# Kernel optimization log

Hardware: AMD Instinct MI355X
Metric: run time of the kernel (lower is better)

## Reference

```python
import jax, jax.numpy as jnp
import numpy as np
from itertools import combinations

B, J, D, H, L, DFF = 2048, 7, 128, 8, 4, 512
TH, GH = 4, 4  # triplet cross-attn heads (min(4,128//32)), group-transformer heads

def _build_static():
    trips = list(combinations(range(J), 3))
    tid = {t: i for i, t in enumerate(trips)}
    member = np.zeros((J, len(trips)), dtype=bool)
    for i, t in enumerate(trips):
        for j in t:
            member[j, i] = True
    isr_l, g1_l, g2_l = [], [], []
    for isr in range(J):
        rem = [j for j in range(J) if j != isr]
        for c in combinations(rem, 3):
            comp = tuple(j for j in rem if j not in c)
            if c < comp:
                isr_l.append(isr); g1_l.append(c); g2_l.append(comp)
    return (np.array(trips), member, np.array(isr_l), np.array(g1_l), np.array(g2_l),
            np.array([tid[t] for t in g1_l]), np.array([tid[t] for t in g2_l]))

TRIPS, MEMBER, ISR_IDX, G1_JETS, G2_JETS, G1_TID, G2_TID = _build_static()
N_ASSIGN = len(ISR_IDX)  # 70
TCA_MASK = np.where(MEMBER, 0.0, -1e9).astype(np.float32)  # (J, 35) jet-restricted mask

def _gelu(x):
    return jax.nn.gelu(x, approximate=False)

def _ln(x, g, b, eps=1e-5):
    mu = x.mean(-1, keepdims=True)
    v = ((x - mu) ** 2).mean(-1, keepdims=True)
    return (x - mu) / jnp.sqrt(v + eps) * g + b

def _attend(q, k, v, nhead, bias=None):
    Bq, Lq, d = q.shape
    Lk = k.shape[1]
    dh = d // nhead
    qh = q.reshape(Bq, Lq, nhead, dh)
    kh = k.reshape(Bq, Lk, nhead, dh)
    vh = v.reshape(Bq, Lk, nhead, dh)
    s = jnp.einsum('bqhd,bkhd->bhqk', qh, kh) / np.float32(np.sqrt(dh))
    if bias is not None:
        s = s + bias
    a = jax.nn.softmax(s, -1)
    return jnp.einsum('bhqk,bkhd->bqhd', a, vh).reshape(Bq, Lq, d)

def _enc_layer(x, Wqkv, bqkv, Wo, bo, g1, b1, g2, b2, W1, bb1, W2, bb2, nhead, bias=None):
    # pre-LN TransformerEncoderLayer (norm_first=True, relu activation, eval mode)
    h = _ln(x, g1, b1)
    q, k, v = jnp.split(h @ Wqkv + bqkv, 3, axis=-1)
    x = x + _attend(q, k, v, nhead, bias) @ Wo + bo
    h2 = _ln(x, g2, b2)
    return x + jax.nn.relu(h2 @ W1 + bb1) @ W2 + bb2

def _feat6(p):
    E, px, py, pz = p[..., 0], p[..., 1], p[..., 2], p[..., 3]
    pt = jnp.sqrt(px ** 2 + py ** 2)
    p3 = jnp.sqrt(pt ** 2 + pz ** 2)
    m = jnp.sqrt(jnp.maximum(E ** 2 - p3 ** 2, 1e-8))
    eta = jnp.arcsinh(pz / jnp.maximum(pt, 1e-8))
    phi = jnp.arctan2(py, px)
    return jnp.stack([m, pt, eta, phi, E, p3], -1)

def _forward(four_momenta, W_in, b_in, pt_w, dr_w, mass_w, enc_Wqkv, enc_bqkv, enc_Wo, enc_bo, enc_g1, enc_b1, enc_g2, enc_b2, enc_W1, enc_bb1, enc_W2, enc_bb2, tca_Wq, tca_bq, tca_Wk, tca_bk, tca_Wv, tca_bv, tca_Wo, tca_bo, tca_g1, tca_b1, tca_W1, tca_bb1, tca_W2, tca_bb2, tca_g2, tca_b2, gt_Wqkv, gt_bqkv, gt_Wo, gt_bo, gt_g1, gt_b1, gt_g2, gt_b2, gt_W1, gt_bb1, gt_W2, gt_bb2, ph_g, ph_b, s_W1, s_b1, s_W2, s_b2, s_W3, s_b3):
    fm = four_momenta
    E, px, py, pz = fm[..., 0], fm[..., 1], fm[..., 2], fm[..., 3]
    pt = jnp.maximum(jnp.sqrt(px ** 2 + py ** 2), 1e-8)
    log_pt = jnp.log(pt)
    eta = jnp.arcsinh(pz / pt)
    phi = jnp.arctan2(py, px)
    m_jet = jnp.sqrt(jnp.maximum(E ** 2 - px ** 2 - py ** 2 - pz ** 2, 1e-8))
    x = jnp.concatenate([fm, jnp.stack([log_pt, eta, phi, m_jet], -1)], -1) @ W_in + b_in

    # fused per-head additive attention biases: pT hierarchy, deltaR, pair invariant mass
    pt_b = log_pt[:, :, None] - log_pt[:, None, :]
    cphi, sphi = px / pt, py / pt
    deta = eta[:, :, None] - eta[:, None, :]
    cdphi = jnp.clip(cphi[:, :, None] * cphi[:, None, :] + sphi[:, :, None] * sphi[:, None, :], -1.0 + 1e-7, 1.0 - 1e-7)
    dr_b = jnp.sqrt(deta ** 2 + jnp.arccos(cdphi) ** 2)
    Es = E[:, :, None] + E[:, None, :]
    ps2 = (px[:, :, None] + px[:, None, :]) ** 2 + (py[:, :, None] + py[:, None, :]) ** 2 + (pz[:, :, None] + pz[:, None, :]) ** 2
    mass_b = 0.5 * jnp.log(jnp.maximum(Es ** 2 - ps2, 1e-8))
    bias = (pt_w[None, :, None, None] * pt_b[:, None] + dr_w[None, :, None, None] * dr_b[:, None] + mass_w[None, :, None, None] * mass_b[:, None])  # (B,H,J,J)

    for i in range(L):
        x = _enc_layer(x, enc_Wqkv[i], enc_bqkv[i], enc_Wo[i], enc_bo[i], enc_g1[i], enc_b1[i], enc_g2[i], enc_b2[i], enc_W1[i], enc_bb1[i], enc_W2[i], enc_bb2[i], H, bias)
    jet_emb = x  # (B, J, D)

    # jet-restricted triplet cross-attention over the C(7,3)=35 triplet bank
    triplet_emb = jet_emb[:, TRIPS].mean(2)  # (B, 35, D)
    q = jet_emb @ tca_Wq + tca_bq
    k = triplet_emb @ tca_Wk + tca_bk
    v = triplet_emb @ tca_Wv + tca_bv
    attn = _attend(q, k, v, TH, jnp.asarray(TCA_MASK)[None, None]) @ tca_Wo + tca_bo
    jet_emb = _ln(jet_emb + attn, tca_g1, tca_b1)
    ff = _gelu(jet_emb @ tca_W1 + tca_bb1) @ tca_W2 + tca_bb2
    jet_emb = _ln(jet_emb + ff, tca_g2, tca_b2)

    # GroupTransformer over all unique 3-jet groups in parallel, mean-pool readout
    nT = len(TRIPS)
    gt_in = jet_emb[:, TRIPS].reshape(B * nT, 3, D)
    gt_out = _enc_layer(gt_in, gt_Wqkv, gt_bqkv, gt_Wo, gt_bo, gt_g1, gt_b1, gt_g2, gt_b2, gt_W1, gt_bb1, gt_W2, gt_bb2, GH)
    group_emb = gt_out.mean(1).reshape(B, nT, D)  # (B, 35, D)

    g1e = group_emb[:, G1_TID]  # (B, 70, D)
    g2e = group_emb[:, G2_TID]
    pair_sum = g1e + g2e
    pair_prod = g1e * g2e
    pair_sqdiff = (g1e - g2e) ** 2
    isr_emb = jet_emb[:, ISR_IDX]  # (B, 70, D)
    event_emb = jnp.broadcast_to(jet_emb.mean(1)[:, None], (B, N_ASSIGN, D))

    p_g1 = fm[:, G1_JETS].sum(2)  # (B, 70, 4)
    p_g2 = fm[:, G2_JETS].sum(2)
    p_isr = fm[:, ISR_IDX]
    physics = jnp.concatenate([_feat6(p_g1), _feat6(p_g2), _feat6(p_isr), _feat6(p_g1 + p_g2)], -1)  # (B,70,24)
    physics = _ln(physics, ph_g, ph_b)

    feats = jnp.concatenate([isr_emb, pair_sum, pair_prod, pair_sqdiff, event_emb, physics], -1)  # (B,70,5D+24)
    h = _gelu(feats @ s_W1 + s_b1)
    h = _gelu(h @ s_W2 + s_b2)
    return (h @ s_W3 + s_b3)[..., 0]  # (B, 70) assignment logits


def setup_inputs():
    key = jax.random.key(0)
    ks = iter(jax.random.split(key, 100))
    def nrm(shape, s=0.02):
        return jax.random.normal(next(ks), shape, jnp.float32) * s
    p3 = jax.random.normal(next(ks), (B, J, 3), jnp.float32) * 50.0
    mm = jnp.abs(jax.random.normal(next(ks), (B, J), jnp.float32)) * 20.0 + 5.0
    E = jnp.sqrt((p3 ** 2).sum(-1) + mm ** 2)
    d = {'four_momenta': jnp.concatenate([E[..., None], p3], -1)}
    d.update(W_in=nrm((8, D)), b_in=jnp.zeros((D,)),
             pt_w=nrm((H,), 0.1), dr_w=nrm((H,), 0.1), mass_w=nrm((H,), 0.1),
             enc_Wqkv=nrm((L, D, 3 * D)), enc_bqkv=jnp.zeros((L, 3 * D)),
             enc_Wo=nrm((L, D, D)), enc_bo=jnp.zeros((L, D)),
             enc_g1=jnp.ones((L, D)), enc_b1=jnp.zeros((L, D)),
             enc_g2=jnp.ones((L, D)), enc_b2=jnp.zeros((L, D)),
             enc_W1=nrm((L, D, DFF)), enc_bb1=jnp.zeros((L, DFF)),
             enc_W2=nrm((L, DFF, D)), enc_bb2=jnp.zeros((L, D)),
             tca_Wq=nrm((D, D)), tca_bq=jnp.zeros((D,)),
             tca_Wk=nrm((D, D)), tca_bk=jnp.zeros((D,)),
             tca_Wv=nrm((D, D)), tca_bv=jnp.zeros((D,)),
             tca_Wo=nrm((D, D)), tca_bo=jnp.zeros((D,)),
             tca_g1=jnp.ones((D,)), tca_b1=jnp.zeros((D,)),
             tca_W1=nrm((D, 2 * D)), tca_bb1=jnp.zeros((2 * D,)),
             tca_W2=nrm((2 * D, D)), tca_bb2=jnp.zeros((D,)),
             tca_g2=jnp.ones((D,)), tca_b2=jnp.zeros((D,)),
             gt_Wqkv=nrm((D, 3 * D)), gt_bqkv=jnp.zeros((3 * D,)),
             gt_Wo=nrm((D, D)), gt_bo=jnp.zeros((D,)),
             gt_g1=jnp.ones((D,)), gt_b1=jnp.zeros((D,)),
             gt_g2=jnp.ones((D,)), gt_b2=jnp.zeros((D,)),
             gt_W1=nrm((D, 2 * D)), gt_bb1=jnp.zeros((2 * D,)),
             gt_W2=nrm((2 * D, D)), gt_bb2=jnp.zeros((D,)),
             ph_g=jnp.ones((24,)), ph_b=jnp.zeros((24,)),
             s_W1=nrm((5 * D + 24, 2 * D)), s_b1=jnp.zeros((2 * D,)),
             s_W2=nrm((2 * D, D)), s_b2=jnp.zeros((D,)),
             s_W3=nrm((D, 1)), s_b3=jnp.zeros((1,)))
    return d


def reference(four_momenta, W_in, b_in, pt_w, dr_w, mass_w, enc_Wqkv, enc_bqkv, enc_Wo, enc_bo, enc_g1, enc_b1, enc_g2, enc_b2, enc_W1, enc_bb1, enc_W2, enc_bb2, tca_Wq, tca_bq, tca_Wk, tca_bk, tca_Wv, tca_bv, tca_Wo, tca_bo, tca_g1, tca_b1, tca_W1, tca_bb1, tca_W2, tca_bb2, tca_g2, tca_b2, gt_Wqkv, gt_bqkv, gt_Wo, gt_bo, gt_g1, gt_b1, gt_g2, gt_b2, gt_W1, gt_bb1, gt_W2, gt_bb2, ph_g, ph_b, s_W1, s_b1, s_W2, s_b2, s_W3, s_b3):
    return _forward(four_momenta, W_in, b_in, pt_w, dr_w, mass_w, enc_Wqkv, enc_bqkv, enc_Wo, enc_bo, enc_g1, enc_b1, enc_g2, enc_b2, enc_W1, enc_bb1, enc_W2, enc_bb2, tca_Wq, tca_bq, tca_Wk, tca_bk, tca_Wv, tca_bv, tca_Wo, tca_bo, tca_g1, tca_b1, tca_W1, tca_bb1, tca_W2, tca_bb2, tca_g2, tca_b2, gt_Wqkv, gt_bqkv, gt_Wo, gt_bo, gt_g1, gt_b1, gt_g2, gt_b2, gt_W1, gt_bb1, gt_W2, gt_bb2, ph_g, ph_b, s_W1, s_b1, s_W2, s_b2, s_W3, s_b3)
```

## Files before the change

kernel.cpp:

```cpp
#include <hip/hip_runtime.h>
#include <hip/hip_bf16.h>
#include <math.h>

typedef __hip_bfloat16 bf16;

constexpr int NB=2048, NJ=7, ND=128, NHD=8, NLYR=4, NFF=512, NTR=35, NAS=70;
constexpr int SD=132, S256=260, S384=388, S512=516;

struct KArgs { const void* p[54]; void* out; const void* flag; };

__device__ __forceinline__ float bfbits(unsigned short s){ return __uint_as_float(((unsigned)s)<<16); }
__device__ __forceinline__ float ldv(const float* p, size_t i){ return p[i]; }
__device__ __forceinline__ float ldv(const bf16* p, size_t i){ return __bfloat162float(p[i]); }
__device__ __forceinline__ void ldv4(const float* p, size_t i, float* o){
  const float4 v=*reinterpret_cast<const float4*>(p+i);
  o[0]=v.x; o[1]=v.y; o[2]=v.z; o[3]=v.w;
}
__device__ __forceinline__ void ldv4(const bf16* p, size_t i, float* o){
  unsigned long long u=*reinterpret_cast<const unsigned long long*>((const unsigned short*)p+i);
  o[0]=bfbits((unsigned short)u);
  o[1]=bfbits((unsigned short)(u>>16));
  o[2]=bfbits((unsigned short)(u>>32));
  o[3]=bfbits((unsigned short)(u>>48));
}
__device__ __forceinline__ void stv(float* p, size_t i, float v){ p[i]=v; }
__device__ __forceinline__ void stv(bf16* p, size_t i, float v){ p[i]=__float2bfloat16(v); }
__device__ __forceinline__ float gelu_f(float x){ return 0.5f*x*(1.0f+erff(x*0.70710678118654752f)); }

__device__ void build_trips(int* tr){
  int n=0;
  for(int a=0;a<NJ;a++)for(int b=a+1;b<NJ;b++)for(int c=b+1;c<NJ;c++){
    tr[n*3+0]=a; tr[n*3+1]=b; tr[n*3+2]=c; n++;
  }
}
__device__ int find_tid(const int* tr,int a,int b,int c){
  for(int t=0;t<NTR;t++) if(tr[t*3]==a&&tr[t*3+1]==b&&tr[t*3+2]==c) return t;
  return 0;
}
__device__ void build_assign(const int* tr,int* isr,int* g1t,int* g2t,int* g1j,int* g2j){
  int n=0;
  for(int is=0;is<NJ;is++){
    int rem[6],m=0;
    for(int j=0;j<NJ;j++) if(j!=is) rem[m++]=j;
    for(int i=0;i<6;i++)for(int jj=i+1;jj<6;jj++)for(int k=jj+1;k<6;k++){
      int c0=rem[i],c1=rem[jj],c2=rem[k];
      int comp[3],q=0;
      for(int r=0;r<6;r++){ int v=rem[r]; if(v!=c0&&v!=c1&&v!=c2) comp[q++]=v; }
      bool lt=(c0<comp[0])||(c0==comp[0]&&(c1<comp[1]||(c1==comp[1]&&c2<comp[2])));
      if(lt){
        isr[n]=is;
        g1j[n*3]=c0; g1j[n*3+1]=c1; g1j[n*3+2]=c2;
        g2j[n*3]=comp[0]; g2j[n*3+1]=comp[1]; g2j[n*3+2]=comp[2];
        g1t[n]=find_tid(tr,c0,c1,c2);
        g2t[n]=find_tid(tr,comp[0],comp[1],comp[2]);
        n++;
      }
    }
  }
}

template<typename T>
__device__ void lnr(const float* src, int ASs, float* dst, int ASd, const T* g, const T* bb,
                    float* mu, float* rs, int rows, int tid, int NT){
  for(int r0=0;r0<rows;r0+=(NT>>5)){
    int row=r0+(tid>>5), lane=tid&31;
    if(row<rows){
      const float* s=src+row*ASs;
      float m=0.f,v=0.f;
      for(int d=lane;d<ND;d+=32){ float t=s[d]; m+=t; v+=t*t; }
      for(int off=16;off>0;off>>=1){ m+=__shfl_down(m,off,32); v+=__shfl_down(v,off,32); }
      if(lane==0){ m*=(1.f/ND); float vv=v*(1.f/ND)-m*m; mu[row]=m; rs[row]=rsqrtf(fmaxf(vv,0.f)+1e-5f); }
    }
    __syncthreads();
  }
  for(int idx=tid; idx<rows*ND; idx+=NT){
    int j=idx>>7, d=idx&127;
    dst[j*ASd+d]=(src[j*ASs+d]-mu[j])*rs[j]*ldv(g,d)+ldv(bb,d);
  }
  __syncthreads();
}

template<typename T>
__device__ void mm4b(const float* a, int ASa, const T* W, const T* bias, float* out, int ASo,
                     int M, int K, int N, int tid, int NT, int act, bool accum, int RB){
  int NQ=N>>2;
  int CGS=NT/RB;
  if(tid<CGS*RB){
    int i=tid%RB, cg0=tid/RB;
    if(i<M){
      const float* ar=a+i*ASa;
      for(int cg=cg0; cg<NQ; cg+=CGS){
        int k4=cg<<2;
        float acc[4];
        if(bias) ldv4(bias,k4,acc);
        else { acc[0]=0.f;acc[1]=0.f;acc[2]=0.f;acc[3]=0.f; }
        for(int d=0; d<K; d++){
          float w[4]; ldv4(W,(size_t)d*N+k4,w);
          float av=ar[d];
          acc[0]+=av*w[0]; acc[1]+=av*w[1]; acc[2]+=av*w[2]; acc[3]+=av*w[3];
        }
        int o=i*ASo+k4;
        #pragma unroll
        for(int j=0;j<4;j++){
          float v=acc[j];
          if(act==1) v=fmaxf(v,0.f); else if(act==2) v=gelu_f(v);
          if(accum) out[o+j]+=v; else out[o+j]=v;
        }
      }
    }
  }
  __syncthreads();
}

__global__ void k_detect(const unsigned short* w, int n, unsigned* flag){
  __shared__ int bad[256];
  int tid=threadIdx.x;
  int my=0;
  for(int i=tid;i<n;i+=256){
    unsigned e=(w[i]>>7)&0xFFu;
    if(e>=134u) my=1;
  }
  bad[tid]=my;
  __syncthreads();
  if(tid==0){
    int any=0; for(int i=0;i<256;i++) any|=bad[i];
    flag[0]= any?1u:0u;
  }
}


template<typename T>
__device__ void phase_embed(const T* fm, const T* Win, const T* bin,
                            const T* ptw, const T* drw, const T* mw,
                            float* xS, float* biasS, float* scratch, int b, int tid, int NT){
  float* fE =scratch+0;  float* fpx=scratch+8;  float* fpy=scratch+16; float* fpz=scratch+24;
  float* flp=scratch+32; float* fet=scratch+40; float* fcp=scratch+48; float* fsp=scratch+56;
  float* fph=scratch+64; float* fms=scratch+72;
  if(tid<NJ){
    size_t base=((size_t)b*NJ+tid)*4;
    float e=ldv(fm,base+0), x_=ldv(fm,base+1), y_=ldv(fm,base+2), z_=ldv(fm,base+3);
    float pt=fmaxf(sqrtf(x_*x_+y_*y_),1e-8f);
    fE[tid]=e; fpx[tid]=x_; fpy[tid]=y_; fpz[tid]=z_;
    flp[tid]=logf(pt);
    fet[tid]=asinhf(z_/pt);
    fph[tid]=atan2f(y_,x_);
    fms[tid]=sqrtf(fmaxf(e*e-x_*x_-y_*y_-z_*z_,1e-8f));
    fcp[tid]=x_/pt; fsp[tid]=y_/pt;
  }
  __syncthreads();
  for(int idx=tid; idx<NJ*ND; idx+=NT){
    int j=idx>>7, d=idx&127;
    float in8[8]={fE[j],fpx[j],fpy[j],fpz[j],flp[j],fet[j],fph[j],fms[j]};
    float acc=ldv(bin,d);
    for(int c=0;c<8;c++) acc += in8[c]*ldv(Win,c*ND+d);
    xS[j*SD+d]=acc;
  }
  for(int idx=tid; idx<NHD*NJ*NJ; idx+=NT){
    int h=idx/49, r=idx%49, i=r/7, jj=r%7;
    float ptb=flp[i]-flp[jj];
    float deta=fet[i]-fet[jj];
    float cd=fcp[i]*fcp[jj]+fsp[i]*fsp[jj];
    cd=fminf(fmaxf(cd,-1.0f+1e-7f),1.0f-1e-7f);
    float ac=acosf(cd);
    float dr=sqrtf(deta*deta+ac*ac);
    float Es=fE[i]+fE[jj];
    float sx=fpx[i]+fpx[jj], sy=fpy[i]+fpy[jj], sz=fpz[i]+fpz[jj];
    float mb=0.5f*logf(fmaxf(Es*Es-(sx*sx+sy*sy+sz*sz),1e-8f));
    biasS[idx]=ldv(ptw,h)*ptb+ldv(drw,h)*dr+ldv(mw,h)*mb;
  }
  __syncthreads();
}

template<typename T>
__device__ void phase_enc(float* xS, const float* biasS, float* P, float* muS, float* rsS,
    const T* eWqkv,const T* ebqkv,const T* eWo,const T* ebo,
    const T* eg1,const T* eb1,const T* eg2,const T* eb2,
    const T* eW1,const T* ebb1,const T* eW2,const T* ebb2, int tid, int NT){
  float* h  =P+0;
  float* qkv=P+924;
  float* att=P+3640;
  float* sb =P+4564;
  float* ff =P+924;
  for(int l=0;l<NLYR;l++){
    lnr(xS,SD,h,SD,eg1+l*ND,eb1+l*ND,muS,rsS,NJ,tid,NT);
    mm4b(h,SD,eWqkv+(size_t)l*ND*3*ND,ebqkv+l*3*ND,qkv,S384,NJ,ND,3*ND,tid,NT,0,false,8);
    for(int idx=tid;idx<NHD*NJ*NJ;idx+=NT){
      int hh=idx/49, r=idx%49, i=r/7, jj=r%7;
      float acc=0.f;
      const float* qr=&qkv[i*S384+hh*16];
      const float* kr=&qkv[jj*S384+128+hh*16];
      for(int d=0;d<16;d++) acc+=qr[d]*kr[d];
      sb[idx]=acc*0.25f+biasS[idx];
    }
    __syncthreads();
    if(tid<NHD*NJ){
      float* s=&sb[tid*7];
      float mx=s[0]; for(int j=1;j<7;j++) mx=fmaxf(mx,s[j]);
      float sm=0.f; for(int j=0;j<7;j++){ s[j]=expf(s[j]-mx); sm+=s[j]; }
      float inv=1.0f/sm; for(int j=0;j<7;j++) s[j]*=inv;
    }
    __syncthreads();
    for(int idx=tid;idx<NJ*ND;idx+=NT){
      int i=idx>>7, d=idx&127, hh=d>>4;
      float acc=0.f;
      for(int j=0;j<7;j++) acc+=sb[(hh*7+i)*7+j]*qkv[j*S384+256+d];
      att[i*SD+d]=acc;
    }
    __syncthreads();
    mm4b(att,SD,eWo+(size_t)l*ND*ND,ebo+l*ND,xS,SD,NJ,ND,ND,tid,NT,0,true,8);
    lnr(xS,SD,h,SD,eg2+l*ND,eb2+l*ND,muS,rsS,NJ,tid,NT);
    mm4b(h,SD,eW1+(size_t)l*ND*NFF,ebb1+l*NFF,ff,S512,NJ,ND,NFF,tid,NT,1,false,8);
    mm4b(ff,S512,eW2+(size_t)l*NFF*ND,ebb2+l*ND,xS,SD,NJ,NFF,ND,tid,NT,0,true,8);
  }
}

template<typename T>
__device__ void trip_proj(const float* xS, const int* trS, const T* W, const T* bias,
                          float* out, int tid, int NT){
  int CGS=NT>>3;
  for(int base=0;base<NTR;base+=8){
    int t=base+(tid&7);
    if(t<NTR){
      int a0=trS[t*3]*SD, a1=trS[t*3+1]*SD, a2=trS[t*3+2]*SD;
      for(int cg=tid>>3; cg<32; cg+=CGS){
        int k4=cg<<2;
        float acc[4]; ldv4(bias,k4,acc);
        for(int c=0;c<ND;c++){
          float tv=(xS[a0+c]+xS[a1+c]+xS[a2+c])*(1.0f/3.0f);
          float w[4]; ldv4(W,(size_t)c*ND+k4,w);
          acc[0]+=tv*w[0]; acc[1]+=tv*w[1]; acc[2]+=tv*w[2]; acc[3]+=tv*w[3];
        }
        int o=t*SD+k4;
        out[o]=acc[0]; out[o+1]=acc[1]; out[o+2]=acc[2]; out[o+3]=acc[3];
      }
    }
  }
  __syncthreads();
}

template<typename T>
__device__ void phase_tca(float* xS, float* P, float* muS, float* rsS, const int* trS,
    const T* tWq,const T* tbq,const T* tWk,const T* tbk,const T* tWv,const T* tbv,
    const T* tWo,const T* tbo,const T* tg1,const T* tb1,const T* tW1,const T* tbb1,
    const T* tW2,const T* tbb2,const T* tg2,const T* tb2, int tid, int NT){
  float* q   =P+0;
  float* kv  =P+924;
  float* sb4 =P+5544;
  float* att2=P+6524;
  float* tff =P+0;
  const float sc=0.17677669529663687f;
  mm4b(xS,SD,tWq,tbq,q,SD,NJ,ND,ND,tid,NT,0,false,8);
  trip_proj(xS,trS,tWk,tbk,kv,tid,NT);
  for(int idx=tid;idx<4*NJ*NTR;idx+=NT){
    int hh=idx/245, r=idx%245, i=r/35, t=r%35;
    float acc=0.f;
    const float* qr=&q[i*SD+hh*32];
    const float* kr=&kv[t*SD+hh*32];
    for(int d=0;d<32;d++) acc+=qr[d]*kr[d];
    bool mem=(trS[t*3]==i||trS[t*3+1]==i||trS[t*3+2]==i);
    sb4[idx]=acc*sc+(mem?0.0f:-1e9f);
  }
  __syncthreads();
  if(tid<4*NJ){
    float* s=&sb4[tid*35];
    float mx=-3e38f; for(int t=0;t<35;t++) mx=fmaxf(mx,s[t]);
    float sm=0.f; for(int t=0;t<35;t++){ s[t]=expf(s[t]-mx); sm+=s[t]; }
    float inv=1.0f/sm; for(int t=0;t<35;t++) s[t]*=inv;
  }
  __syncthreads();
  trip_proj(xS,trS,tWv,tbv,kv,tid,NT);
  for(int idx=tid;idx<NJ*ND;idx+=NT){
    int i=idx>>7, d=idx&127, hh=d>>5;
    float acc=0.f;
    for(int t=0;t<35;t++) acc+=sb4[(hh*7+i)*35+t]*kv[t*SD+d];
    att2[i*SD+d]=acc;
  }
  __syncthreads();
  mm4b(att2,SD,tWo,tbo,xS,SD,NJ,ND,ND,tid,NT,0,true,8);
  lnr(xS,SD,xS,SD,tg1,tb1,muS,rsS,NJ,tid,NT);
  mm4b(xS,SD,tW1,tbb1,tff,S256,NJ,ND,2*ND,tid,NT,2,false,8);
  mm4b(tff,S256,tW2,tbb2,xS,SD,NJ,2*ND,ND,tid,NT,0,true,8);
  lnr(xS,SD,xS,SD,tg2,tb2,muS,rsS,NJ,tid,NT);
}


template<typename T>
__global__ __launch_bounds__(256) void k_front(KArgs A, unsigned want, float* X2, float* EVT){
  if(((const unsigned*)A.flag)[0]!=want) return;
  int b=blockIdx.x, tid=threadIdx.x;
  __shared__ float xS[NJ*SD];
  __shared__ float biasS[NHD*NJ*NJ];
  __shared__ float P[7448];
  __shared__ float muS[16], rsS[16];
  __shared__ int trS[NTR*3];
  if(tid==0) build_trips(trS);
  __syncthreads();
  phase_embed((const T*)A.p[0],(const T*)A.p[1],(const T*)A.p[2],
              (const T*)A.p[3],(const T*)A.p[4],(const T*)A.p[5],xS,biasS,P,b,tid,256);
  phase_enc(xS,biasS,P,muS,rsS,
    (const T*)A.p[6],(const T*)A.p[7],(const T*)A.p[8],(const T*)A.p[9],
    (const T*)A.p[10],(const T*)A.p[11],(const T*)A.p[12],(const T*)A.p[13],
    (const T*)A.p[14],(const T*)A.p[15],(const T*)A.p[16],(const T*)A.p[17],tid,256);
  phase_tca(xS,P,muS,rsS,trS,
    (const T*)A.p[18],(const T*)A.p[19],(const T*)A.p[20],(const T*)A.p[21],
    (const T*)A.p[22],(const T*)A.p[23],(const T*)A.p[24],(const T*)A.p[25],
    (const T*)A.p[26],(const T*)A.p[27],(const T*)A.p[28],(const T*)A.p[29],
    (const T*)A.p[30],(const T*)A.p[31],(const T*)A.p[32],(const T*)A.p[33],tid,256);
  for(int idx=tid;idx<NJ*ND;idx+=256) X2[(size_t)b*NJ*ND+idx]=xS[(idx>>7)*SD+(idx&127)];
  if(tid<ND){
    float s=0.f; for(int j=0;j<NJ;j++) s+=xS[j*SD+tid];
    EVT[(size_t)b*ND+tid]=s*(1.0f/NJ);
  }
}

template<typename T>
__global__ __launch_bounds__(256) void k_gt(KArgs A, unsigned want, const float* X2, float* GRP){
  if(((const unsigned*)A.flag)[0]!=want) return;
  const T* gWqkv=(const T*)A.p[34]; const T* gbqkv=(const T*)A.p[35];
  const T* gWo  =(const T*)A.p[36]; const T* gbo  =(const T*)A.p[37];
  const T* gg1  =(const T*)A.p[38]; const T* gb1  =(const T*)A.p[39];
  const T* gg2  =(const T*)A.p[40]; const T* gb2  =(const T*)A.p[41];
  const T* gW1  =(const T*)A.p[42]; const T* gbb1 =(const T*)A.p[43];
  const T* gW2  =(const T*)A.p[44]; const T* gbb2 =(const T*)A.p[45];
  int b=blockIdx.x/12, ch=blockIdx.x%12, tid=threadIdx.x;
  int c0=ch*3, tc=(NTR-c0)<3?(NTR-c0):3;
  int ntok=3*tc;
  __shared__ float jets[NJ*SD];
  __shared__ float xg[9*SD];
  __shared__ float hg[9*SD];
  __shared__ float qkvg[9*S384];
  __shared__ float sbg[108];
  __shared__ float muS[16], rsS[16];
  __shared__ int trS[NTR*3];
  if(tid==0) build_trips(trS);
  for(int idx=tid;idx<NJ*ND;idx+=256) jets[(idx>>7)*SD+(idx&127)]=X2[(size_t)b*NJ*ND+idx];
  __syncthreads();
  const float sc=0.17677669529663687f;
  for(int idx=tid;idx<ntok*ND;idx+=256){
    int s=idx>>7, d=idx&127; int t=c0+s/3, r=s%3;
    xg[s*SD+d]=jets[trS[t*3+r]*SD+d];
  }
  __syncthreads();
  lnr(xg,SD,hg,SD,gg1,gb1,muS,rsS,ntok,tid,256);
  mm4b(hg,SD,gWqkv,gbqkv,qkvg,S384,ntok,ND,3*ND,tid,256,0,false,9);
  for(int idx=tid;idx<tc*36;idx+=256){
    int s=idx/36, r=idx%36, hh=r/9, p=r%9, i=p/3, j=p%3;
    float acc=0.f;
    const float* qr=&qkvg[(s*3+i)*S384+hh*32];
    const float* kr=&qkvg[(s*3+j)*S384+128+hh*32];
    for(int d=0;d<32;d++) acc+=qr[d]*kr[d];
    sbg[idx]=acc*sc;
  }
  __syncthreads();
  for(int q2=tid;q2<tc*12;q2+=256){
    int s=q2/12, r2=q2%12;
    float* base=&sbg[s*36+(r2/3)*9+(r2%3)*3];
    float mx=fmaxf(base[0],fmaxf(base[1],base[2]));
    float e0=expf(base[0]-mx),e1=expf(base[1]-mx),e2=expf(base[2]-mx);
    float inv=1.0f/(e0+e1+e2);
    base[0]=e0*inv; base[1]=e1*inv; base[2]=e2*inv;
  }
  __syncthreads();
  for(int idx=tid;idx<ntok*ND;idx+=256){
    int sr=idx>>7, d=idx&127; int s=sr/3, i=sr%3, hh=d>>5;
    float acc=0.f;
    for(int j=0;j<3;j++) acc+=sbg[s*36+hh*9+i*3+j]*qkvg[(s*3+j)*S384+256+d];
    hg[sr*SD+d]=acc;
  }
  __syncthreads();
  mm4b(hg,SD,gWo,gbo,xg,SD,ntok,ND,ND,tid,256,0,true,9);
  lnr(xg,SD,hg,SD,gg2,gb2,muS,rsS,ntok,tid,256);
  mm4b(hg,SD,gW1,gbb1,qkvg,S256,ntok,ND,2*ND,tid,256,1,false,9);
  mm4b(qkvg,S256,gW2,gbb2,xg,SD,ntok,2*ND,ND,tid,256,0,true,9);
  for(int idx=tid;idx<tc*ND;idx+=256){
    int s=idx>>7, d=idx&127;
    GRP[((size_t)b*NTR+c0+s)*ND+d]=
      (xg[(s*3)*SD+d]+xg[(s*3+1)*SD+d]+xg[(s*3+2)*SD+d])*(1.0f/3.0f);
  }
}

template<typename T>
__global__ __launch_bounds__(512) void k_score(KArgs A, unsigned want,
    const float* X2, const float* EVT, const float* GRP){
  if(((const unsigned*)A.flag)[0]!=want) return;
  const T* fm =(const T*)A.p[0];
  const T* phg=(const T*)A.p[46]; const T* phb=(const T*)A.p[47];
  const T* sW1=(const T*)A.p[48]; const T* sb1=(const T*)A.p[49];
  const T* sW2=(const T*)A.p[50]; const T* sb2=(const T*)A.p[51];
  const T* sW3=(const T*)A.p[52]; const T* sb3=(const T*)A.p[53];
  T* OUT=(T*)A.out;
  int b=blockIdx.x, tid=threadIdx.x;
  int ar=tid&7, cg=tid>>3;

  __shared__ float POOL[12472];
  float* grpP=POOL;
  float* Ws  =POOL+4680;
  float* h2t =POOL+4680;
  float* h1c =POOL+8776;
  float* Fc  =POOL+10096;
  float* jets=POOL+10096;
  __shared__ float physAll[72*24];
  __shared__ float isrc[7*260];
  __shared__ float evtc[256];
  __shared__ float evtS[128];
  __shared__ float fmvS[28];
  __shared__ int trS[105];
  __shared__ int isrS[72], g1tS[72], g2tS[72], g1jS[216], g2jS[216];

  if(tid==0){
    build_trips(trS); build_assign(trS,isrS,g1tS,g2tS,g1jS,g2jS);
    for(int a=70;a<72;a++){
      isrS[a]=0; g1tS[a]=0; g2tS[a]=0;
      for(int r=0;r<3;r++){ g1jS[a*3+r]=0; g2jS[a*3+r]=0; }
    }
  }
  for(int idx=tid;idx<NTR*ND;idx+=512) grpP[(idx>>7)*132+(idx&127)]=GRP[(size_t)b*NTR*ND+idx];
  for(int idx=tid;idx<NJ*ND;idx+=512) jets[idx]=X2[(size_t)b*NJ*ND+idx];
  if(tid<ND) evtS[tid]=EVT[(size_t)b*ND+tid];
  if(tid>=128&&tid<128+NJ*4){ int q=tid-128; fmvS[q]=ldv(fm,(size_t)b*NJ*4+q); }
  __syncthreads();

  {
    int i=tid&7, k4=(tid>>3)<<2;
    const float* src=(i<7)?(jets+i*ND):evtS;
    size_t rb=(i<7)?0:(size_t)4*ND;
    float acc[4];
    if(i==7) ldv4(sb1,k4,acc); else { acc[0]=0.f;acc[1]=0.f;acc[2]=0.f;acc[3]=0.f; }
    for(int d=0;d<ND;d++){
      float w[4]; ldv4(sW1,(rb+d)*2*ND+k4,w);
      float av=src[d];
      acc[0]+=av*w[0]; acc[1]+=av*w[1]; acc[2]+=av*w[2]; acc[3]+=av*w[3];
    }
    if(i<7){ int o=i*260+k4; isrc[o]=acc[0]; isrc[o+1]=acc[1]; isrc[o+2]=acc[2]; isrc[o+3]=acc[3]; }
    else   { evtc[k4]=acc[0]; evtc[k4+1]=acc[1]; evtc[k4+2]=acc[2]; evtc[k4+3]=acc[3]; }
  }
  if(tid<72*4){
    int a=tid>>2, g=tid&3;
    float* o=&physAll[a*24+g*6];
    if(a<NAS){
      float p[4];
      #pragma unroll
      for(int c=0;c<4;c++){
        float v;
        if(g==0)      v=fmvS[g1jS[a*3]*4+c]+fmvS[g1jS[a*3+1]*4+c]+fmvS[g1jS[a*3+2]*4+c];
        else if(g==1) v=fmvS[g2jS[a*3]*4+c]+fmvS[g2jS[a*3+1]*4+c]+fmvS[g2jS[a*3+2]*4+c];
        else if(g==2) v=fmvS[isrS[a]*4+c];
        else          v=fmvS[g1jS[a*3]*4+c]+fmvS[g1jS[a*3+1]*4+c]+fmvS[g1jS[a*3+2]*4+c]
                       +fmvS[g2jS[a*3]*4+c]+fmvS[g2jS[a*3+1]*4+c]+fmvS[g2jS[a*3+2]*4+c];
        p[c]=v;
      }
      float E=p[0], x_=p[1], y_=p[2], z_=p[3];
      float pt=sqrtf(x_*x_+y_*y_);
      float p3=sqrtf(pt*pt+z_*z_);
      float m =sqrtf(fmaxf(E*E-p3*p3,1e-8f));
      float eta=asinhf(z_/fmaxf(pt,1e-8f));
      float ph=atan2f(y_,x_);
      o[0]=m; o[1]=pt; o[2]=eta; o[3]=ph; o[4]=E; o[5]=p3;
    } else { o[0]=0;o[1]=0;o[2]=0;o[3]=0;o[4]=0;o[5]=0; }
  }
  __syncthreads();
  if(tid<72){
    float* o=&physAll[tid*24];
    float m=0.f; for(int c=0;c<24;c++) m+=o[c]; m*=(1.0f/24.0f);
    float v=0.f; for(int c=0;c<24;c++){ float t=o[c]-m; v+=t*t; } v*=(1.0f/24.0f);
    float r=rsqrtf(v+1e-5f);
    for(int c=0;c<24;c++) o[c]=(o[c]-m)*r*ldv(phg,c)+ldv(phb,c);
  }
  __syncthreads();

  for(int t=0;t<2;t++){
    int tbase=t*40;
    int ns=(t==0)?5:4;
    float acc[5][4];
    #pragma unroll
    for(int s=0;s<5;s++){ acc[s][0]=0.f;acc[s][1]=0.f;acc[s][2]=0.f;acc[s][3]=0.f; }

    for(int kc=0;kc<408;kc+=16){
      int csz=(408-kc)<16?(408-kc):16;
      for(int idx4=tid*4; idx4<csz*256; idx4+=2048){
        int d=idx4>>8, n=idx4&255;
        int c=kc+d;
        size_t r=(c<384)? (size_t)(ND+c) : (size_t)(5*ND+(c-384));
        float w[4]; ldv4(sW1,r*2*ND+n,w);
        Ws[d*256+n]=w[0]; Ws[d*256+n+1]=w[1]; Ws[d*256+n+2]=w[2]; Ws[d*256+n+3]=w[3];
      }
      for(int idx=tid; idx<72*16; idx+=512){
        int a=idx>>4, d=idx&15;
        if(d<csz){
          int c=kc+d;
          float f;
          if(c<384){
            int cc=c&127, kind=c>>7;
            float u=grpP[g1tS[a]*132+cc], w=grpP[g2tS[a]*132+cc];
            f=(kind==0)?(u+w):(kind==1)?(u*w):(u-w)*(u-w);
          } else f=physAll[a*24+(c-384)];
          Fc[a*17+d]=f;
        }
      }
      __syncthreads();
      for(int d=0;d<csz;d++){
        float w[4]; 
        const float* wp=&Ws[d*256+(cg<<2)];
        w[0]=wp[0]; w[1]=wp[1]; w[2]=wp[2]; w[3]=wp[3];
        #pragma unroll
        for(int s=0;s<5;s++){
          if(s<ns){
            float f=Fc[(tbase+ar+8*s)*17+d];
            acc[s][0]+=f*w[0]; acc[s][1]+=f*w[1]; acc[s][2]+=f*w[2]; acc[s][3]+=f*w[3];
          }
        }
      }
      __syncthreads();
    }
    float h1r[5][4];
    #pragma unroll
    for(int s=0;s<5;s++){
      if(s<ns){
        int a=tbase+ar+8*s;
        int ir=isrS[a];
        #pragma unroll
        for(int j=0;j<4;j++){
          int k=(cg<<2)+j;
          h1r[s][j]=gelu_f(acc[s][j]+evtc[k]+isrc[ir*260+k]);
        }
      } else { h1r[s][0]=0;h1r[s][1]=0;h1r[s][2]=0;h1r[s][3]=0; }
    }

    float acc2[5][4];
    {
      float b2v[4]; int k4b=(cg&31)<<2; ldv4(sb2,k4b,b2v);
      #pragma unroll
      for(int s=0;s<5;s++){ acc2[s][0]=b2v[0];acc2[s][1]=b2v[1];acc2[s][2]=b2v[2];acc2[s][3]=b2v[3]; }
    }
    for(int fc=0;fc<256;fc+=32){
      if(cg>=(fc>>2)&&cg<(fc>>2)+8){
        int dcol=(cg<<2)-fc;
        #pragma unroll
        for(int s=0;s<5;s++){
          if(s<ns){
            int al=ar+8*s;
            h1c[al*33+dcol]  =h1r[s][0];
            h1c[al*33+dcol+1]=h1r[s][1];
            h1c[al*33+dcol+2]=h1r[s][2];
            h1c[al*33+dcol+3]=h1r[s][3];
          }
        }
      }
      for(int idx4=tid*4; idx4<32*128; idx4+=2048){
        int d=idx4>>7, n=idx4&127;
        float w[4]; ldv4(sW2,(size_t)(fc+d)*128+n,w);
        Ws[d*128+n]=w[0]; Ws[d*128+n+1]=w[1]; Ws[d*128+n+2]=w[2]; Ws[d*128+n+3]=w[3];
      }
      __syncthreads();
      if(cg<32){
        for(int d=0;d<32;d++){
          const float* wp=&Ws[d*128+(cg<<2)];
          float w0=wp[0],w1=wp[1],w2=wp[2],w3=wp[3];
          #pragma unroll
          for(int s=0;s<5;s++){
            if(s<ns){
              float f=h1c[(ar+8*s)*33+d];
              acc2[s][0]+=f*w0; acc2[s][1]+=f*w1; acc2[s][2]+=f*w2; acc2[s][3]+=f*w3;
            }
          }
        }
      }
      __syncthreads();
    }
    if(cg<32){
      int k4=cg<<2;
      #pragma unroll
      for(int s=0;s<5;s++){
        if(s<ns){
          int al=ar+8*s;
          h2t[al*129+k4]  =gelu_f(acc2[s][0]);
          h2t[al*129+k4+1]=gelu_f(acc2[s][1]);
          h2t[al*129+k4+2]=gelu_f(acc2[s][2]);
          h2t[al*129+k4+3]=gelu_f(acc2[s][3]);
        }
      }
    }
    __syncthreads();
    {
      int widx=tid>>6, lane=tid&63;
      int nal=(t==0)?40:30;
      for(int s2=0;s2<5;s2++){
        int al=widx+8*s2;
        if(al<nal){
          float part=h2t[al*129+lane]*ldv(sW3,lane)+h2t[al*129+64+lane]*ldv(sW3,64+lane);
          for(int off=32;off>0;off>>=1) part+=__shfl_down(part,off,64);
          if(lane==0) stv(OUT,(size_t)b*NAS+tbase+al,part+ldv(sb3,0));
        }
      }
    }
    __syncthreads();
  }
}

extern "C" void kernel_launch(void* const* d_in, const int* in_sizes, int n_in,
                              void* d_out, int out_size, void* d_ws, size_t ws_size,
                              hipStream_t stream){
  KArgs A;
  for(int i=0;i<54;i++) A.p[i]=d_in[i];
  A.out=d_out;
  A.flag=d_ws;

  float* ws=(float*)d_ws;
  float* X2  = ws+16;
  float* EVT = X2 + (size_t)NB*NJ*ND;
  float* GRP = EVT + (size_t)NB*ND;

  k_detect<<<1,256,0,stream>>>((const unsigned short*)d_in[1],1024,(unsigned*)d_ws);

  k_front<bf16> <<<NB,256,0,stream>>>(A,0u,X2,EVT);
  k_front<float><<<NB,256,0,stream>>>(A,1u,X2,EVT);
  k_gt<bf16>    <<<NB*12,256,0,stream>>>(A,0u,X2,GRP);
  k_gt<float>   <<<NB*12,256,0,stream>>>(A,1u,X2,GRP);
  k_score<bf16> <<<NB,512,0,stream>>>(A,0u,X2,EVT,GRP);
  k_score<float><<<NB,512,0,stream>>>(A,1u,X2,EVT,GRP);
}
```

Baseline: 7.639 ms.

## Stage weight tiles in shared memory for per-event matmuls and enlarge group-transformer chunks

Replaces the per-thread global-memory weight streaming matmul with a staged version. The block cooperatively loads K-chunks of the weight matrix into a shared buffer, and each thread then accumulates several output slots from it. Triplet projections get the same treatment. The group-transformer kernel now handles 6 triplets per block instead of 3, halving the block count so each staged weight tile is reused across more tokens. The cost is more shared memory per block, which lowers occupancy, plus extra barriers per chunk.

After: 9.998 ms. 1.31x slower.

```diff
diff --git a/kernel.cpp b/kernel.cpp
--- a/kernel.cpp
+++ b/kernel.cpp
@@ -80,33 +80,103 @@
   __syncthreads();
 }
 
-template<typename T>
-__device__ void mm4b(const float* a, int ASa, const T* W, const T* bias, float* out, int ASo,
-                     int M, int K, int N, int tid, int NT, int act, bool accum, int RB){
-  int NQ=N>>2;
-  int CGS=NT/RB;
-  if(tid<CGS*RB){
-    int i=tid%RB, cg0=tid/RB;
-    if(i<M){
-      const float* ar=a+i*ASa;
-      for(int cg=cg0; cg<NQ; cg+=CGS){
-        int k4=cg<<2;
-        float acc[4];
-        if(bias) ldv4(bias,k4,acc);
-        else { acc[0]=0.f;acc[1]=0.f;acc[2]=0.f;acc[3]=0.f; }
-        for(int d=0; d<K; d++){
-          float w[4]; ldv4(W,(size_t)d*N+k4,w);
-          float av=ar[d];
-          acc[0]+=av*w[0]; acc[1]+=av*w[1]; acc[2]+=av*w[2]; acc[3]+=av*w[3];
-        }
-        int o=i*ASo+k4;
-        #pragma unroll
-        for(int j=0;j<4;j++){
-          float v=acc[j];
-          if(act==1) v=fmaxf(v,0.f); else if(act==2) v=gelu_f(v);
-          if(accum) out[o+j]+=v; else out[o+j]=v;
-        }
-      }
+template<int N, int KC, int MAXSL, typename T>
+__device__ void mm_stage(const float* a, int ASa, const T* W, const T* bias,
+                         float* out, int ASo, int M, int K, float* Ws,
+                         int tid, int NT, int act, bool accum){
+  constexpr int NQ=N>>2;
+  int slots=M*NQ;
+  int rj[MAXSL], c4[MAXSL];
+  float acc[MAXSL][4];
+  #pragma unroll
+  for(int j=0;j<MAXSL;j++){
+    int s=tid+j*NT;
+    if(s<slots){
+      rj[j]=s%M; c4[j]=(s/M)<<2;
+      if(bias) ldv4(bias,c4[j],acc[j]);
+      else { acc[j][0]=0.f;acc[j][1]=0.f;acc[j][2]=0.f;acc[j][3]=0.f; }
+    }
+  }
+  for(int kc=0;kc<K;kc+=KC){
+    for(int i4=tid*4;i4<KC*N;i4+=NT*4){
+      int d=i4/N, n=i4-d*N;
+      float w[4]; ldv4(W,(size_t)(kc+d)*N+n,w);
+      *(float4*)&Ws[d*N+n]=make_float4(w[0],w[1],w[2],w[3]);
+    }
+    __syncthreads();
+    #pragma unroll
+    for(int j=0;j<MAXSL;j++){
+      int s=tid+j*NT;
+      if(s<slots){
+        const float* ap=a+rj[j]*ASa+kc;
+        const float* wp=Ws+c4[j];
+        for(int d=0;d<KC;d++){
+          float av=ap[d];
+          float4 wv=*(const float4*)(wp+d*N);
+          acc[j][0]+=av*wv.x; acc[j][1]+=av*wv.y; acc[j][2]+=av*wv.z; acc[j][3]+=av*wv.w;
+        }
+      }
+    }
+    __syncthreads();
+  }
+  #pragma unroll
+  for(int j=0;j<MAXSL;j++){
+    int s=tid+j*NT;
+    if(s<slots){
+      int o=rj[j]*ASo+c4[j];
+      #pragma unroll
+      for(int q=0;q<4;q++){
+        float v=acc[j][q];
+        if(act==1) v=fmaxf(v,0.f); else if(act==2) v=gelu_f(v);
+        if(accum) out[o+q]+=v; else out[o+q]=v;
+      }
+    }
+  }
+  __syncthreads();
+}
+
+template<int MAXSL, typename T>
+__device__ void mm_stage_trip(const float* xS, const int* trS, const T* W, const T* bias,
+                              float* out, float* Ws, int tid, int NT){
+  const int slots=NTR*32;
+  int a0[MAXSL],a1[MAXSL],a2[MAXSL],c4[MAXSL],tt[MAXSL];
+  float acc[MAXSL][4];
+  #pragma unroll
+  for(int j=0;j<MAXSL;j++){
+    int s=tid+j*NT;
+    if(s<slots){
+      int t=s%NTR; tt[j]=t; c4[j]=(s/NTR)<<2;
+      a0[j]=trS[t*3]*SD; a1[j]=trS[t*3+1]*SD; a2[j]=trS[t*3+2]*SD;
+      ldv4(bias,c4[j],acc[j]);
+    }
+  }
+  for(int kc=0;kc<128;kc+=16){
+    for(int i4=tid*4;i4<16*128;i4+=NT*4){
+      int d=i4>>7, n=i4&127;
+      float w[4]; ldv4(W,(size_t)(kc+d)*128+n,w);
+      *(float4*)&Ws[d*128+n]=make_float4(w[0],w[1],w[2],w[3]);
+    }
+    __syncthreads();
+    #pragma unroll
+    for(int j=0;j<MAXSL;j++){
+      int s=tid+j*NT;
+      if(s<slots){
+        const float* wp=Ws+c4[j];
+        for(int d=0;d<16;d++){
+          float tv=(xS[a0[j]+kc+d]+xS[a1[j]+kc+d]+xS[a2[j]+kc+d])*(1.0f/3.0f);
+          float4 wv=*(const float4*)(wp+d*128);
+          acc[j][0]+=tv*wv.x; acc[j][1]+=tv*wv.y; acc[j][2]+=tv*wv.z; acc[j][3]+=tv*wv.w;
+        }
+      }
+    }
+    __syncthreads();
+  }
+  #pragma unroll
+  for(int j=0;j<MAXSL;j++){
+    int s=tid+j*NT;
+    if(s<slots){
+      int o=tt[j]*SD+c4[j];
+      out[o]=acc[j][0]; out[o+1]=acc[j][1]; out[o+2]=acc[j][2]; out[o+3]=acc[j][3];
     }
   }
   __syncthreads();
@@ -172,7 +242,8 @@
 }
 
 template<typename T>
-__device__ void phase_enc(float* xS, const float* biasS, float* P, float* muS, float* rsS,
+__device__ void phase_enc(float* xS, const float* biasS, float* P, float* Ws,
+    float* muS, float* rsS,
     const T* eWqkv,const T* ebqkv,const T* eWo,const T* ebo,
     const T* eg1,const T* eb1,const T* eg2,const T* eb2,
     const T* eW1,const T* ebb1,const T* eW2,const T* ebb2, int tid, int NT){
@@ -183,7 +254,7 @@
   float* ff =P+924;
   for(int l=0;l<NLYR;l++){
     lnr(xS,SD,h,SD,eg1+l*ND,eb1+l*ND,muS,rsS,NJ,tid,NT);
-    mm4b(h,SD,eWqkv+(size_t)l*ND*3*ND,ebqkv+l*3*ND,qkv,S384,NJ,ND,3*ND,tid,NT,0,false,8);
+    mm_stage<384,16,3>(h,SD,eWqkv+(size_t)l*ND*3*ND,ebqkv+l*3*ND,qkv,S384,NJ,ND,Ws,tid,NT,0,false);
     for(int idx=tid;idx<NHD*NJ*NJ;idx+=NT){
       int hh=idx/49, r=idx%49, i=r/7, jj=r%7;
       float acc=0.f;
@@ -207,39 +278,15 @@
       att[i*SD+d]=acc;
     }
     __syncthreads();
-    mm4b(att,SD,eWo+(size_t)l*ND*ND,ebo+l*ND,xS,SD,NJ,ND,ND,tid,NT,0,true,8);
+    mm_stage<128,16,1>(att,SD,eWo+(size_t)l*ND*ND,ebo+l*ND,xS,SD,NJ,ND,Ws,tid,NT,0,true);
     lnr(xS,SD,h,SD,eg2+l*ND,eb2+l*ND,muS,rsS,NJ,tid,NT);
-    mm4b(h,SD,eW1+(size_t)l*ND*NFF,ebb1+l*NFF,ff,S512,NJ,ND,NFF,tid,NT,1,false,8);
-    mm4b(ff,S512,eW2+(size_t)l*NFF*ND,ebb2+l*ND,xS,SD,NJ,NFF,ND,tid,NT,0,true,8);
+    mm_stage<512,8,4>(h,SD,eW1+(size_t)l*ND*NFF,ebb1+l*NFF,ff,S512,NJ,ND,Ws,tid,NT,1,false);
+    mm_stage<128,16,1>(ff,S512,eW2+(size_t)l*NFF*ND,ebb2+l*ND,xS,SD,NJ,NFF,Ws,tid,NT,0,true);
   }
 }
 
 template<typename T>
-__device__ void trip_proj(const float* xS, const int* trS, const T* W, const T* bias,
-                          float* out, int tid, int NT){
-  int CGS=NT>>3;
-  for(int base=0;base<NTR;base+=8){
-    int t=base+(tid&7);
-    if(t<NTR){
-      int a0=trS[t*3]*SD, a1=trS[t*3+1]*SD, a2=trS[t*3+2]*SD;
-      for(int cg=tid>>3; cg<32; cg+=CGS){
-        int k4=cg<<2;
-        float acc[4]; ldv4(bias,k4,acc);
-        for(int c=0;c<ND;c++){
-          float tv=(xS[a0+c]+xS[a1+c]+xS[a2+c])*(1.0f/3.0f);
-          float w[4]; ldv4(W,(size_t)c*ND+k4,w);
-          acc[0]+=tv*w[0]; acc[1]+=tv*w[1]; acc[2]+=tv*w[2]; acc[3]+=tv*w[3];
-        }
-        int o=t*SD+k4;
-        out[o]=acc[0]; out[o+1]=acc[1]; out[o+2]=acc[2]; out[o+3]=acc[3];
-      }
-    }
-  }
-  __syncthreads();
-}
-
-template<typename T>
-__device__ void phase_tca(float* xS, float* P, float* muS, float* rsS, const int* trS,
+__device__ void phase_tca(float* xS, float* P, float* Ws, float* muS, float* rsS, const int* trS,
     const T* tWq,const T* tbq,const T* tWk,const T* tbk,const T* tWv,const T* tbv,
     const T* tWo,const T* tbo,const T* tg1,const T* tb1,const T* tW1,const T* tbb1,
     const T* tW2,const T* tbb2,const T* tg2,const T* tb2, int tid, int NT){
@@ -249,8 +296,8 @@
   float* att2=P+6524;
   float* tff =P+0;
   const float sc=0.17677669529663687f;
-  mm4b(xS,SD,tWq,tbq,q,SD,NJ,ND,ND,tid,NT,0,false,8);
-  trip_proj(xS,trS,tWk,tbk,kv,tid,NT);
+  mm_stage<128,16,1>(xS,SD,tWq,tbq,q,SD,NJ,ND,Ws,tid,NT,0,false);
+  mm_stage_trip<5>(xS,trS,tWk,tbk,kv,Ws,tid,NT);
   for(int idx=tid;idx<4*NJ*NTR;idx+=NT){
     int hh=idx/245, r=idx%245, i=r/35, t=r%35;
     float acc=0.f;
@@ -268,7 +315,7 @@
     float inv=1.0f/sm; for(int t=0;t<35;t++) s[t]*=inv;
   }
   __syncthreads();
-  trip_proj(xS,trS,tWv,tbv,kv,tid,NT);
+  mm_stage_trip<5>(xS,trS,tWv,tbv,kv,Ws,tid,NT);
   for(int idx=tid;idx<NJ*ND;idx+=NT){
     int i=idx>>7, d=idx&127, hh=d>>5;
     float acc=0.f;
@@ -276,10 +323,10 @@
     att2[i*SD+d]=acc;
   }
   __syncthreads();
-  mm4b(att2,SD,tWo,tbo,xS,SD,NJ,ND,ND,tid,NT,0,true,8);
+  mm_stage<128,16,1>(att2,SD,tWo,tbo,xS,SD,NJ,ND,Ws,tid,NT,0,true);
   lnr(xS,SD,xS,SD,tg1,tb1,muS,rsS,NJ,tid,NT);
-  mm4b(xS,SD,tW1,tbb1,tff,S256,NJ,ND,2*ND,tid,NT,2,false,8);
-  mm4b(tff,S256,tW2,tbb2,xS,SD,NJ,2*ND,ND,tid,NT,0,true,8);
+  mm_stage<256,16,2>(xS,SD,tW1,tbb1,tff,S256,NJ,ND,Ws,tid,NT,2,false);
+  mm_stage<128,16,1>(tff,S256,tW2,tbb2,xS,SD,NJ,2*ND,Ws,tid,NT,0,true);
   lnr(xS,SD,xS,SD,tg2,tb2,muS,rsS,NJ,tid,NT);
 }
 
@@ -291,17 +338,18 @@
   __shared__ float xS[NJ*SD];
   __shared__ float biasS[NHD*NJ*NJ];
   __shared__ float P[7448];
+  __shared__ float WsS[6144];
   __shared__ float muS[16], rsS[16];
   __shared__ int trS[NTR*3];
   if(tid==0) build_trips(trS);
   __syncthreads();
   phase_embed((const T*)A.p[0],(const T*)A.p[1],(const T*)A.p[2],
               (const T*)A.p[3],(const T*)A.p[4],(const T*)A.p[5],xS,biasS,P,b,tid,256);
-  phase_enc(xS,biasS,P,muS,rsS,
+  phase_enc(xS,biasS,P,WsS,muS,rsS,
     (const T*)A.p[6],(const T*)A.p[7],(const T*)A.p[8],(const T*)A.p[9],
     (const T*)A.p[10],(const T*)A.p[11],(const T*)A.p[12],(const T*)A.p[13],
     (const T*)A.p[14],(const T*)A.p[15],(const T*)A.p[16],(const T*)A.p[17],tid,256);
-  phase_tca(xS,P,muS,rsS,trS,
+  phase_tca(xS,P,WsS,muS,rsS,trS,
     (const T*)A.p[18],(const T*)A.p[19],(const T*)A.p[20],(const T*)A.p[21],
     (const T*)A.p[22],(const T*)A.p[23],(const T*)A.p[24],(const T*)A.p[25],
     (const T*)A.p[26],(const T*)A.p[27],(const T*)A.p[28],(const T*)A.p[29],
@@ -322,15 +370,16 @@
   const T* gg2  =(const T*)A.p[40]; const T* gb2  =(const T*)A.p[41];
   const T* gW1  =(const T*)A.p[42]; const T* gbb1 =(const T*)A.p[43];
   const T* gW2  =(const T*)A.p[44]; const T* gbb2 =(const T*)A.p[45];
-  int b=blockIdx.x/12, ch=blockIdx.x%12, tid=threadIdx.x;
-  int c0=ch*3, tc=(NTR-c0)<3?(NTR-c0):3;
+  int b=blockIdx.x/6, ch=blockIdx.x%6, tid=threadIdx.x;
+  int c0=ch*6, tc=(NTR-c0)<6?(NTR-c0):6;
   int ntok=3*tc;
   __shared__ float jets[NJ*SD];
-  __shared__ float xg[9*SD];
-  __shared__ float hg[9*SD];
-  __shared__ float qkvg[9*S384];
-  __shared__ float sbg[108];
-  __shared__ float muS[16], rsS[16];
+  __shared__ float xg[18*SD];
+  __shared__ float hg[18*SD];
+  __shared__ float qkvg[18*S384];
+  __shared__ float WsS[6144];
+  __shared__ float sbg[216];
+  __shared__ float muS[24], rsS[24];
   __shared__ int trS[NTR*3];
   if(tid==0) build_trips(trS);
   for(int idx=tid;idx<NJ*ND;idx+=256) jets[(idx>>7)*SD+(idx&127)]=X2[(size_t)b*NJ*ND+idx];
@@ -342,7 +391,7 @@
   }
   __syncthreads();
   lnr(xg,SD,hg,SD,gg1,gb1,muS,rsS,ntok,tid,256);
-  mm4b(hg,SD,gWqkv,gbqkv,qkvg,S384,ntok,ND,3*ND,tid,256,0,false,9);
+  mm_stage<384,16,7>(hg,SD,gWqkv,gbqkv,qkvg,S384,ntok,ND,WsS,tid,256,0,false);
   for(int idx=tid;idx<tc*36;idx+=256){
     int s=idx/36, r=idx%36, hh=r/9, p=r%9, i=p/3, j=p%3;
     float acc=0.f;
@@ -368,10 +417,10 @@
     hg[sr*SD+d]=acc;
   }
   __syncthreads();
-  mm4b(hg,SD,gWo,gbo,xg,SD,ntok,ND,ND,tid,256,0,true,9);
+  mm_stage<128,16,3>(hg,SD,gWo,gbo,xg,SD,ntok,ND,WsS,tid,256,0,true);
   lnr(xg,SD,hg,SD,gg2,gb2,muS,rsS,ntok,tid,256);
-  mm4b(hg,SD,gW1,gbb1,qkvg,S256,ntok,ND,2*ND,tid,256,1,false,9);
-  mm4b(qkvg,S256,gW2,gbb2,xg,SD,ntok,2*ND,ND,tid,256,0,true,9);
+  mm_stage<256,16,5>(hg,SD,gW1,gbb1,qkvg,S256,ntok,ND,WsS,tid,256,1,false);
+  mm_stage<128,16,3>(qkvg,S256,gW2,gbb2,xg,SD,ntok,2*ND,WsS,tid,256,0,true);
   for(int idx=tid;idx<tc*ND;idx+=256){
     int s=idx>>7, d=idx&127;
     GRP[((size_t)b*NTR+c0+s)*ND+d]=
@@ -499,14 +548,13 @@
       }
       __syncthreads();
       for(int d=0;d<csz;d++){
-        float w[4]; 
         const float* wp=&Ws[d*256+(cg<<2)];
-        w[0]=wp[0]; w[1]=wp[1]; w[2]=wp[2]; w[3]=wp[3];
+        float w0=wp[0],w1=wp[1],w2=wp[2],w3=wp[3];
         #pragma unroll
         for(int s=0;s<5;s++){
           if(s<ns){
             float f=Fc[(tbase+ar+8*s)*17+d];
-            acc[s][0]+=f*w[0]; acc[s][1]+=f*w[1]; acc[s][2]+=f*w[2]; acc[s][3]+=f*w[3];
+            acc[s][0]+=f*w0; acc[s][1]+=f*w1; acc[s][2]+=f*w2; acc[s][3]+=f*w3;
           }
         }
       }
@@ -614,8 +662,8 @@
 
   k_front<bf16> <<<NB,256,0,stream>>>(A,0u,X2,EVT);
   k_front<float><<<NB,256,0,stream>>>(A,1u,X2,EVT);
-  k_gt<bf16>    <<<NB*12,256,0,stream>>>(A,0u,X2,GRP);
-  k_gt<float>   <<<NB*12,256,0,stream>>>(A,1u,X2,GRP);
+  k_gt<bf16>    <<<NB*6,256,0,stream>>>(A,0u,X2,GRP);
+  k_gt<float>   <<<NB*6,256,0,stream>>>(A,1u,X2,GRP);
   k_score<bf16> <<<NB,512,0,stream>>>(A,0u,X2,EVT,GRP);
   k_score<float><<<NB,512,0,stream>>>(A,1u,X2,EVT,GRP);
 }
```
